# Performance work log

Measured on AMD Instinct MI355X. Metric: run time of the kernel, lower is better.

The kernel has to match this reference:

```python
import jax, jax.numpy as jnp
import numpy as np

N_NODES = 50000
N_EDGES = 800000
NUM_GRAPHS = 512


def setup_inputs() -> dict:
    key = jax.random.key(0)
    ks = jax.random.split(key, 8)
    x = jax.random.normal(ks[0], (N_NODES, 128), dtype=jnp.float32)
    W1 = jax.random.normal(ks[1], (128, 128), dtype=jnp.float32) * (1.0 / np.sqrt(128))
    b1 = jnp.zeros((128,), dtype=jnp.float32)
    W2 = jax.random.normal(ks[2], (128, 64), dtype=jnp.float32) * (1.0 / np.sqrt(128))
    b2 = jnp.zeros((64,), dtype=jnp.float32)
    edge_index = jax.random.randint(ks[3], (2, N_EDGES), 0, N_NODES, dtype=jnp.int32)
    batch = jnp.sort(jax.random.randint(ks[4], (N_NODES,), 0, NUM_GRAPHS, dtype=jnp.int32))
    return {"x": x, "W1": W1, "b1": b1, "W2": W2, "b2": b2,
            "edge_index": edge_index, "batch": batch}


def reference(x, W1, b1, W2, b2, edge_index, batch):
    N = x.shape[0]
    # add self-loops (PyG GCNConv default)
    loop = jnp.arange(N, dtype=edge_index.dtype)
    src = jnp.concatenate([edge_index[0], loop])  # [E+N] message sources (x_j)
    dst = jnp.concatenate([edge_index[1], loop])  # [E+N] aggregation targets
    # symmetric degree normalization: deg^{-1/2}[src] * deg^{-1/2}[dst]
    deg = jax.ops.segment_sum(jnp.ones_like(dst, dtype=x.dtype), dst, num_segments=N)
    dinv = jnp.where(deg > 0, jax.lax.rsqrt(jnp.maximum(deg, 1.0)), 0.0)
    norm = (dinv[src] * dinv[dst])[:, None]  # [E+N, 1]

    def gcn_conv(h, W, b):
        hw = h @ W                                    # [N, d_out]
        msg = hw[src] * norm                          # gather + scale, [E+N, d_out]
        return jax.ops.segment_sum(msg, dst, num_segments=N) + b

    h = jax.nn.relu(gcn_conv(x, W1, b1))
    z = gcn_conv(h, W2, b2)
    # global_mean_pool over batch segment ids
    sums = jax.ops.segment_sum(z, batch, num_segments=NUM_GRAPHS)
    cnt = jax.ops.segment_sum(jnp.ones((N,), z.dtype), batch, num_segments=NUM_GRAPHS)
    return sums / jnp.maximum(cnt, 1.0)[:, None]
```

## Files before the change

kernel.cpp:

```cpp
#include <hip/hip_runtime.h>
#include <hip/hip_fp16.h>


typedef _Float16 half8 __attribute__((ext_vector_type(8)));
typedef float    f32x4 __attribute__((ext_vector_type(4)));
union U4H8 { uint4 u; half8 h; };

__global__ void count_wt_kernel(const int* __restrict__ ei, int E, int N,
                                int* __restrict__ cnt,
                                const float* __restrict__ W1, const float* __restrict__ W2,
                                __half* __restrict__ wt1, __half* __restrict__ wt2) {
    int i = blockIdx.x * blockDim.x + threadIdx.x;
    int total = E + N;
    if (i < total) {
        int d = (i < E) ? ei[E + i] : (i - E);
        atomicAdd(&cnt[d], 1);
        return;
    }
    int id = i - total;
    const float* W; __half* dst; int M_, n, c8;
    if (id < 2048)      { W = W1; dst = wt1; M_ = 128; n = id >> 4;          c8 = id & 15; }
    else if (id < 3072) { W = W2; dst = wt2; M_ = 64;  n = (id - 2048) >> 4; c8 = id & 15; }
    else return;
    union { __half h[8]; uint4 u; } pk;
#pragma unroll
    for (int j = 0; j < 8; ++j) pk.h[j] = __float2half(W[(c8 * 8 + j) * M_ + n]);
    *(uint4*)((char*)dst + n * 256 + ((c8 ^ (n & 15)) << 4)) = pk.u;
}

__global__ void scan_block_kernel(const int* __restrict__ cnt, int N,
                                  int* __restrict__ excl, int* __restrict__ partial) {
    __shared__ int tmp[1024];
    int t = threadIdx.x;
    int i = blockIdx.x * 1024 + t;
    int v = (i < N) ? cnt[i] : 0;
    tmp[t] = v;
    __syncthreads();
    for (int off = 1; off < 1024; off <<= 1) {
        int add = (t >= off) ? tmp[t - off] : 0;
        __syncthreads();
        tmp[t] += add;
        __syncthreads();
    }
    if (i < N) excl[i] = tmp[t] - v;
    if (t == 1023) partial[blockIdx.x] = tmp[1023];
}

__global__ void scan_partial_kernel(int* __restrict__ partial, int nb) {
    if (blockIdx.x == 0 && threadIdx.x == 0) {
        int run = 0;
        for (int i = 0; i < nb; ++i) { int v = partial[i]; partial[i] = run; run += v; }
    }
}

__global__ void finalize_kernel(int* __restrict__ indptr, int* __restrict__ cursor,
                                const int* __restrict__ cnt, float* __restrict__ dinv,
                                const int* __restrict__ partial, int N, int total) {
    int i = blockIdx.x * blockDim.x + threadIdx.x;
    if (i < N) {
        int v = indptr[i] + partial[i >> 10];
        indptr[i] = v;
        cursor[i] = v;
        dinv[i] = rsqrtf((float)cnt[i]);
    }
    if (i == 0) indptr[N] = total;
}

__global__ void fill_kernel(const int* __restrict__ ei, int E, int N,
                            int* __restrict__ cursor, ushort* __restrict__ csr) {
    int i = blockIdx.x * blockDim.x + threadIdx.x;
    if (i >= E + N) return;
    int s, d;
    if (i < E) { s = ei[i]; d = ei[E + i]; }
    else       { s = i - E; d = s; }
    int pos = atomicAdd(&cursor[d], 1);
    csr[pos] = (ushort)s;
}

template<int M, bool HALF_IN>
__global__ __launch_bounds__(256) void gemm_mfma_kernel(const void* __restrict__ Xv,
                                                        const __half* __restrict__ wt,
                                                        __half* __restrict__ out, int NT) {
    __shared__ __align__(16) char wlds[M * 256];
    int tid = threadIdx.x;
    {
        const uint4* src = (const uint4*)wt;
        uint4* dstv = (uint4*)wlds;
#pragma unroll
        for (int i = 0; i < (M * 16) / 256; ++i) dstv[tid + i * 256] = src[tid + i * 256];
    }
    __syncthreads();

    int wid  = tid >> 6;
    int lane = tid & 63;
    int rt   = blockIdx.x * 4 + wid;
    if (rt >= NT) return;
    int l15 = lane & 15, l4 = lane >> 4;

    half8 a[4];
    if (HALF_IN) {
        const char* X = (const char*)Xv;
        size_t rb = (size_t)(rt * 16 + l15) * 256;
#pragma unroll
        for (int c = 0; c < 4; ++c) {
            U4H8 u; u.u = *(const uint4*)(X + rb + c * 64 + l4 * 16);
            a[c] = u.h;
        }
    } else {
        const float* X = (const float*)Xv;
        size_t rb = (size_t)(rt * 16 + l15) * 128;
#pragma unroll
        for (int c = 0; c < 4; ++c) {
            const float* p = X + rb + c * 32 + l4 * 8;
            float4 f0 = *(const float4*)p;
            float4 f1 = *(const float4*)(p + 4);
            half8 h;
            h[0] = (_Float16)f0.x; h[1] = (_Float16)f0.y;
            h[2] = (_Float16)f0.z; h[3] = (_Float16)f0.w;
            h[4] = (_Float16)f1.x; h[5] = (_Float16)f1.y;
            h[6] = (_Float16)f1.z; h[7] = (_Float16)f1.w;
            a[c] = h;
        }
    }

    constexpr int CT = M / 16;
    f32x4 acc[CT];
#pragma unroll
    for (int t = 0; t < CT; ++t) acc[t] = (f32x4){0.f, 0.f, 0.f, 0.f};

#pragma unroll
    for (int c = 0; c < 4; ++c) {
#pragma unroll
        for (int t = 0; t < CT; ++t) {
            int n  = t * 16 + l15;
            int c8 = c * 4 + l4;
            U4H8 b; b.u = *(const uint4*)(wlds + n * 256 + ((c8 ^ (n & 15)) << 4));
            acc[t] = __builtin_amdgcn_mfma_f32_16x16x32_f16(a[c], b.h, acc[t], 0, 0, 0);
        }
    }

#pragma unroll
    for (int t = 0; t < CT; ++t) {
#pragma unroll
        for (int r = 0; r < 4; ++r) {
            int row = rt * 16 + l4 * 4 + r;
            out[(size_t)row * M + t * 16 + l15] = __float2half(acc[t][r]);
        }
    }
}

__device__ __forceinline__ void acc_h8(f32x4& a0, f32x4& a1, uint4 r, float w) {
    __half2* h = (__half2*)&r;
    float2 f0 = __half22float2(h[0]);
    float2 f1 = __half22float2(h[1]);
    float2 f2 = __half22float2(h[2]);
    float2 f3 = __half22float2(h[3]);
    a0[0] = fmaf(f0.x, w, a0[0]); a0[1] = fmaf(f0.y, w, a0[1]);
    a0[2] = fmaf(f1.x, w, a0[2]); a0[3] = fmaf(f1.y, w, a0[3]);
    a1[0] = fmaf(f2.x, w, a1[0]); a1[1] = fmaf(f2.y, w, a1[1]);
    a1[2] = fmaf(f3.x, w, a1[2]); a1[3] = fmaf(f3.y, w, a1[3]);
}

__global__ void agg128_relu_kernel(const uint4* __restrict__ hw,
                                   const int* __restrict__ indptr,
                                   const ushort* __restrict__ csr,
                                   const float* __restrict__ dinv,
                                   const float* __restrict__ b1,
                                   uint4* __restrict__ outh, int N) {
    int gid  = (blockIdx.x * blockDim.x + threadIdx.x) >> 4;
    int lane = threadIdx.x & 15;
    if (gid >= N) return;
    int beg = indptr[gid], end = indptr[gid + 1];
    float dl = dinv[gid];
    f32x4 a0 = (f32x4){0.f, 0.f, 0.f, 0.f};
    f32x4 a1 = (f32x4){0.f, 0.f, 0.f, 0.f};
    int e = beg;
    for (; e + 4 <= end; e += 4) {
        int s0 = csr[e], s1 = csr[e + 1], s2 = csr[e + 2], s3 = csr[e + 3];
        float w0 = dinv[s0] * dl, w1 = dinv[s1] * dl;
        float w2 = dinv[s2] * dl, w3 = dinv[s3] * dl;
        uint4 r0 = hw[(size_t)s0 * 16 + lane];
        uint4 r1 = hw[(size_t)s1 * 16 + lane];
        uint4 r2 = hw[(size_t)s2 * 16 + lane];
        uint4 r3 = hw[(size_t)s3 * 16 + lane];
        acc_h8(a0, a1, r0, w0);
        acc_h8(a0, a1, r1, w1);
        acc_h8(a0, a1, r2, w2);
        acc_h8(a0, a1, r3, w3);
    }
    for (; e < end; ++e) {
        int s0 = csr[e];
        float w0 = dinv[s0] * dl;
        uint4 r0 = hw[(size_t)s0 * 16 + lane];
        acc_h8(a0, a1, r0, w0);
    }
    float4 b0 = *(const float4*)(b1 + lane * 8);
    float4 b1v = *(const float4*)(b1 + lane * 8 + 4);
    float o0 = fmaxf(a0[0] + b0.x, 0.f), o1 = fmaxf(a0[1] + b0.y, 0.f);
    float o2 = fmaxf(a0[2] + b0.z, 0.f), o3 = fmaxf(a0[3] + b0.w, 0.f);
    float o4 = fmaxf(a1[0] + b1v.x, 0.f), o5 = fmaxf(a1[1] + b1v.y, 0.f);
    float o6 = fmaxf(a1[2] + b1v.z, 0.f), o7 = fmaxf(a1[3] + b1v.w, 0.f);
    __half2 p0 = __floats2half2_rn(o0, o1);
    __half2 p1 = __floats2half2_rn(o2, o3);
    __half2 p2 = __floats2half2_rn(o4, o5);
    __half2 p3 = __floats2half2_rn(o6, o7);
    uint4 pk;
    pk.x = *(unsigned int*)&p0; pk.y = *(unsigned int*)&p1;
    pk.z = *(unsigned int*)&p2; pk.w = *(unsigned int*)&p3;
    outh[(size_t)gid * 16 + lane] = pk;
}

__global__ void agg64_kernel(const uint4* __restrict__ hw,
                             const int* __restrict__ indptr,
                             const ushort* __restrict__ csr,
                             const float* __restrict__ dinv,
                             float* __restrict__ outz, int N) {
    int gid  = (blockIdx.x * blockDim.x + threadIdx.x) >> 3;
    int lane = threadIdx.x & 7;
    if (gid >= N) return;
    int beg = indptr[gid], end = indptr[gid + 1];
    float dl = dinv[gid];
    f32x4 a0 = (f32x4){0.f, 0.f, 0.f, 0.f};
    f32x4 a1 = (f32x4){0.f, 0.f, 0.f, 0.f};
    int e = beg;
    for (; e + 4 <= end; e += 4) {
        int s0 = csr[e], s1 = csr[e + 1], s2 = csr[e + 2], s3 = csr[e + 3];
        float w0 = dinv[s0] * dl, w1 = dinv[s1] * dl;
        float w2 = dinv[s2] * dl, w3 = dinv[s3] * dl;
        uint4 r0 = hw[(size_t)s0 * 8 + lane];
        uint4 r1 = hw[(size_t)s1 * 8 + lane];
        uint4 r2 = hw[(size_t)s2 * 8 + lane];
        uint4 r3 = hw[(size_t)s3 * 8 + lane];
        acc_h8(a0, a1, r0, w0);
        acc_h8(a0, a1, r1, w1);
        acc_h8(a0, a1, r2, w2);
        acc_h8(a0, a1, r3, w3);
    }
    for (; e < end; ++e) {
        int s0 = csr[e];
        float w0 = dinv[s0] * dl;
        uint4 r0 = hw[(size_t)s0 * 8 + lane];
        acc_h8(a0, a1, r0, w0);
    }
    float* zp = outz + (size_t)gid * 64 + lane * 8;
    *(f32x4*)zp       = a0;
    *(f32x4*)(zp + 4) = a1;
}

__device__ __forceinline__ int lower_bound_i(const int* a, int n, int key) {
    int lo = 0, hi = n;
    while (lo < hi) {
        int mid = (lo + hi) >> 1;
        if (a[mid] < key) lo = mid + 1; else hi = mid;
    }
    return lo;
}

__global__ void pool_kernel(const float* __restrict__ z, const int* __restrict__ batch,
                            const float* __restrict__ b2, float* __restrict__ out,
                            int N, int G) {
    __shared__ float red[4][64];
    int g  = blockIdx.x;
    int c  = threadIdx.x & 63;
    int rr = threadIdx.x >> 6;
    int s  = lower_bound_i(batch, N, g);
    int e  = lower_bound_i(batch, N, g + 1);
    float acc = 0.f;
    for (int n = s + rr; n < e; n += 4) acc += z[n * 64 + c];
    red[rr][c] = acc;
    __syncthreads();
    if (rr == 0) {
        float a = red[0][c] + red[1][c] + red[2][c] + red[3][c];
        int cnt = e - s;
        out[g * 64 + c] = (cnt > 0) ? (a / (float)cnt + b2[c]) : 0.f;
    }
}

extern "C" void kernel_launch(void* const* d_in, const int* in_sizes, int n_in,
                              void* d_out, int out_size, void* d_ws, size_t ws_size,
                              hipStream_t stream) {
    const float* x  = (const float*)d_in[0];
    const float* W1 = (const float*)d_in[1];
    const float* b1 = (const float*)d_in[2];
    const float* W2 = (const float*)d_in[3];
    const float* b2 = (const float*)d_in[4];
    const int*   ei = (const int*)d_in[5];
    const int*   batch = (const int*)d_in[6];

    const int N = in_sizes[6];
    const int E = in_sizes[5] / 2;
    const int Gnum = out_size / 64;
    const int total = E + N;

    char* ws = (char*)d_ws;
    size_t off = 0;
    auto alloc = [&](size_t bytes) {
        size_t o = off;
        off = (off + bytes + 255) & ~(size_t)255;
        return (void*)(ws + o);
    };
    int*    cnt     = (int*)   alloc((size_t)N * 4);
    int*    indptr  = (int*)   alloc((size_t)(N + 1) * 4);
    int*    cursor  = (int*)   alloc((size_t)N * 4);
    float*  dinv    = (float*) alloc((size_t)N * 4);
    int*    partial = (int*)   alloc(256 * 4);
    ushort* csr     = (ushort*)alloc((size_t)total * 2);
    __half* wt1     = (__half*)alloc(128 * 256);
    __half* wt2     = (__half*)alloc(64 * 256);
    __half* bufA    = (__half*)alloc((size_t)N * 128 * 2);
    __half* bufB    = (__half*)alloc((size_t)N * 128 * 2);
    float*  bufZ    = (float*) alloc((size_t)N * 64 * 4);
    (void)ws_size; (void)n_in;

    hipMemsetAsync(cnt, 0, (size_t)N * 4, stream);

    int tb = 256;
    int cg = (total + 3072 + tb - 1) / tb;
    count_wt_kernel<<<cg, tb, 0, stream>>>(ei, E, N, cnt, W1, W2, wt1, wt2);

    int nb = (N + 1023) / 1024;
    scan_block_kernel<<<nb, 1024, 0, stream>>>(cnt, N, indptr, partial);
    scan_partial_kernel<<<1, 1, 0, stream>>>(partial, nb);
    finalize_kernel<<<(N + tb - 1) / tb, tb, 0, stream>>>(indptr, cursor, cnt, dinv,
                                                          partial, N, total);
    fill_kernel<<<(total + tb - 1) / tb, tb, 0, stream>>>(ei, E, N, cursor, csr);

    const int NT = (N + 15) / 16;
    gemm_mfma_kernel<128, false><<<(NT + 3) / 4, 256, 0, stream>>>(x, wt1, bufA, NT);
    agg128_relu_kernel<<<(N * 16 + 255) / 256, 256, 0, stream>>>(
        (const uint4*)bufA, indptr, csr, dinv, b1, (uint4*)bufB, N);

    gemm_mfma_kernel<64, true><<<(NT + 3) / 4, 256, 0, stream>>>(bufB, wt2, bufA, NT);
    agg64_kernel<<<(N * 8 + 255) / 256, 256, 0, stream>>>(
        (const uint4*)bufA, indptr, csr, dinv, bufZ, N);

    pool_kernel<<<Gnum, 256, 0, stream>>>(bufZ, batch, b2, (float*)d_out, N, Gnum);
}
```

Before: 243.3 us.

## Partition count and fill atomics by destination range across block groups

The degree-count and CSR-fill kernels now assign each block one of eight destination-node ranges, selected by block index modulo eight, and use grid-stride loops. Each block reads every edge but performs atomics only for destinations in its range. Because consecutive blocks cover different ranges, the intent is to spread atomic traffic across memory channels and keep each range's counters local to cache. The trade-off is that every edge index is read eight times, and the weight-transpose work moves into twelve dedicated tail blocks.

Result: no change. 243.2 us (-0.0%).

```diff
diff --git a/kernel.cpp b/kernel.cpp
--- a/kernel.cpp
+++ b/kernel.cpp
@@ -5,27 +5,37 @@
 typedef _Float16 half8 __attribute__((ext_vector_type(8)));
 typedef float    f32x4 __attribute__((ext_vector_type(4)));
 union U4H8 { uint4 u; half8 h; };
+
+#define NPART 8
 
 __global__ void count_wt_kernel(const int* __restrict__ ei, int E, int N,
                                 int* __restrict__ cnt,
                                 const float* __restrict__ W1, const float* __restrict__ W2,
                                 __half* __restrict__ wt1, __half* __restrict__ wt2) {
-    int i = blockIdx.x * blockDim.x + threadIdx.x;
+    int bid = blockIdx.x;
+    int nbc = gridDim.x - 12;
+    if (bid >= nbc) {
+        int id = (bid - nbc) * blockDim.x + threadIdx.x;
+        const float* W; __half* dst; int M_, n, c8;
+        if (id < 2048)      { W = W1; dst = wt1; M_ = 128; n = id >> 4;          c8 = id & 15; }
+        else if (id < 3072) { W = W2; dst = wt2; M_ = 64;  n = (id - 2048) >> 4; c8 = id & 15; }
+        else return;
+        union { __half h[8]; uint4 u; } pk;
+#pragma unroll
+        for (int j = 0; j < 8; ++j) pk.h[j] = __float2half(W[(c8 * 8 + j) * M_ + n]);
+        *(uint4*)((char*)dst + n * 256 + ((c8 ^ (n & 15)) << 4)) = pk.u;
+        return;
+    }
+    int part = bid & (NPART - 1);
+    int bsub = bid >> 3;
+    int nb   = nbc >> 3;
+    int dlo  = (int)(((long long)N * part) >> 3);
+    int dhi  = (int)(((long long)N * (part + 1)) >> 3);
     int total = E + N;
-    if (i < total) {
+    for (int i = bsub * blockDim.x + threadIdx.x; i < total; i += nb * blockDim.x) {
         int d = (i < E) ? ei[E + i] : (i - E);
-        atomicAdd(&cnt[d], 1);
-        return;
-    }
-    int id = i - total;
-    const float* W; __half* dst; int M_, n, c8;
-    if (id < 2048)      { W = W1; dst = wt1; M_ = 128; n = id >> 4;          c8 = id & 15; }
-    else if (id < 3072) { W = W2; dst = wt2; M_ = 64;  n = (id - 2048) >> 4; c8 = id & 15; }
-    else return;
-    union { __half h[8]; uint4 u; } pk;
-#pragma unroll
-    for (int j = 0; j < 8; ++j) pk.h[j] = __float2half(W[(c8 * 8 + j) * M_ + n]);
-    *(uint4*)((char*)dst + n * 256 + ((c8 ^ (n & 15)) << 4)) = pk.u;
+        if (d >= dlo && d < dhi) atomicAdd(&cnt[d], 1);
+    }
 }
 
 __global__ void scan_block_kernel(const int* __restrict__ cnt, int N,
@@ -68,13 +78,20 @@
 
 __global__ void fill_kernel(const int* __restrict__ ei, int E, int N,
                             int* __restrict__ cursor, ushort* __restrict__ csr) {
-    int i = blockIdx.x * blockDim.x + threadIdx.x;
-    if (i >= E + N) return;
-    int s, d;
-    if (i < E) { s = ei[i]; d = ei[E + i]; }
-    else       { s = i - E; d = s; }
-    int pos = atomicAdd(&cursor[d], 1);
-    csr[pos] = (ushort)s;
+    int part = blockIdx.x & (NPART - 1);
+    int bsub = blockIdx.x >> 3;
+    int nb   = gridDim.x >> 3;
+    int dlo  = (int)(((long long)N * part) >> 3);
+    int dhi  = (int)(((long long)N * (part + 1)) >> 3);
+    int total = E + N;
+    for (int i = bsub * blockDim.x + threadIdx.x; i < total; i += nb * blockDim.x) {
+        int d = (i < E) ? ei[E + i] : (i - E);
+        if (d >= dlo && d < dhi) {
+            int s = (i < E) ? ei[i] : d;
+            int pos = atomicAdd(&cursor[d], 1);
+            csr[pos] = (ushort)s;
+        }
+    }
 }
 
 template<int M, bool HALF_IN>
@@ -315,15 +332,15 @@
     hipMemsetAsync(cnt, 0, (size_t)N * 4, stream);
 
     int tb = 256;
-    int cg = (total + 3072 + tb - 1) / tb;
-    count_wt_kernel<<<cg, tb, 0, stream>>>(ei, E, N, cnt, W1, W2, wt1, wt2);
+    const int NBC = 2048;
+    count_wt_kernel<<<NBC + 12, tb, 0, stream>>>(ei, E, N, cnt, W1, W2, wt1, wt2);
 
     int nb = (N + 1023) / 1024;
     scan_block_kernel<<<nb, 1024, 0, stream>>>(cnt, N, indptr, partial);
     scan_partial_kernel<<<1, 1, 0, stream>>>(partial, nb);
     finalize_kernel<<<(N + tb - 1) / tb, tb, 0, stream>>>(indptr, cursor, cnt, dinv,
                                                           partial, N, total);
-    fill_kernel<<<(total + tb - 1) / tb, tb, 0, stream>>>(ei, E, N, cursor, csr);
+    fill_kernel<<<NBC, tb, 0, stream>>>(ei, E, N, cursor, csr);
 
     const int NT = (N + 15) / 16;
     gemm_mfma_kernel<128, false><<<(NT + 3) / 4, 256, 0, stream>>>(x, wt1, bufA, NT);
```
